# Performance work log

Measured on AMD Instinct MI355X. Metric: run time of the kernel, lower is better.

The kernel has to match this reference:

```python
import jax, jax.numpy as jnp
import numpy as np

NUM_HEADS = 16
HEAD_DIM = 80
DIM = NUM_HEADS * HEAD_DIM
SEQ = 2048
SCALE = HEAD_DIM ** -0.5


def rotate_half(x):
    x1, x2 = jnp.split(x, 2, axis=-1)
    return jnp.concatenate((-x2, x1), axis=-1)


def setup_inputs() -> dict:
    key = jax.random.key(0)
    ks = jax.random.split(key, 8)
    hidden_states = jax.random.normal(ks[0], (SEQ, DIM), dtype=jnp.float32)
    cu_seqlens = jnp.array([0, SEQ], dtype=jnp.int32)  # unused by the math
    # rotary embeddings for head_dim
    inv_freq = 1.0 / (10000.0 ** (jnp.arange(0, HEAD_DIM // 2, dtype=jnp.float32) / (HEAD_DIM // 2)))
    freqs = jnp.outer(jnp.arange(SEQ, dtype=jnp.float32), inv_freq)  # [S, hd/2]
    emb = jnp.concatenate((freqs, freqs), axis=-1)  # [S, hd]
    cos = jnp.cos(emb)
    sin = jnp.sin(emb)
    w_qkv = jax.random.normal(ks[1], (3 * DIM, DIM), dtype=jnp.float32) * (DIM ** -0.5)
    b_qkv = jax.random.normal(ks[2], (3 * DIM,), dtype=jnp.float32) * 0.02
    w_proj = jax.random.normal(ks[3], (DIM, DIM), dtype=jnp.float32) * (DIM ** -0.5)
    b_proj = jax.random.normal(ks[4], (DIM,), dtype=jnp.float32) * 0.02
    return {"hidden_states": hidden_states, "cu_seqlens": cu_seqlens, "cos": cos,
            "sin": sin, "w_qkv": w_qkv, "b_qkv": b_qkv, "w_proj": w_proj, "b_proj": b_proj}


def reference(hidden_states, cu_seqlens, cos, sin, w_qkv, b_qkv, w_proj, b_proj):
    S = hidden_states.shape[0]
    qkv = hidden_states @ w_qkv.T + b_qkv  # [S, 3*D]
    qkv = qkv.reshape(S, 3, NUM_HEADS, HEAD_DIM)
    q, k, v = qkv[:, 0], qkv[:, 1], qkv[:, 2]  # each [S, H, hd]
    c = cos[:, None, :]  # [S, 1, hd]
    s = sin[:, None, :]
    q = q * c + rotate_half(q) * s
    k = k * c + rotate_half(k) * s
    # SDPA, non-causal: [H, S, S]
    scores = jnp.einsum('shd,thd->hst', q, k) * SCALE
    attn = jax.nn.softmax(scores, axis=-1)
    out = jnp.einsum('hst,thd->shd', attn, v).reshape(S, DIM)
    return out @ w_proj.T + b_proj
```

## Files before the change

### kernel.cpp

```cpp
#include <hip/hip_runtime.h>


#define SEQLEN   2048
#define DIMM     1280
#define NHEADS   16
#define HD       80
#define HDP      96
#define QKV_N    3840
#define NSPLIT   2
#define KVSPAN   (SEQLEN / NSPLIT)
#define QSCALE_LOG2E 0.16130083587064776f

#define KSTRIDE  104
#define VSTRIDE  72
#define PSTRIDE  72

#define EXP2F(x) __builtin_amdgcn_exp2f(x)

#define GLD16(gptr, lptr)                                                      \
    __builtin_amdgcn_global_load_lds(                                          \
        (const __attribute__((address_space(1))) void*)(gptr),                 \
        (__attribute__((address_space(3))) void*)(lptr), 16, 0, 0)

typedef float f32x4 __attribute__((ext_vector_type(4)));
typedef _Float16 half8 __attribute__((ext_vector_type(8)));
typedef _Float16 half4 __attribute__((ext_vector_type(4)));

static __device__ __forceinline__ f32x4 mfma_16x16x32(half8 a, half8 b, f32x4 c) {
    return __builtin_amdgcn_mfma_f32_16x16x32_f16(a, b, c, 0, 0, 0);
}

__global__ void cast_f32_f16(const float* __restrict__ src,
                             _Float16* __restrict__ dst, int n4) {
    int i = blockIdx.x * blockDim.x + threadIdx.x;
    if (i < n4) {
        const float4 v = ((const float4*)src)[i];
        half4 h;
        h.x = (_Float16)v.x; h.y = (_Float16)v.y;
        h.z = (_Float16)v.z; h.w = (_Float16)v.w;
        ((half4*)dst)[i] = h;
    }
}

template<bool OUT_F16>
__global__ __launch_bounds__(256, 2)
void gemm_bt(const _Float16* __restrict__ A, const _Float16* __restrict__ B,
             const float* __restrict__ bias, void* __restrict__ Cout,
             int M, int N, int K) {
    __shared__ __align__(16) _Float16 As[128 * 32];
    __shared__ __align__(16) _Float16 Bs[128 * 32];
    const int tid  = threadIdx.x;
    const int lane = tid & 63;
    const int wave = tid >> 6;
    const int l15  = lane & 15;
    const int quad = lane >> 4;
    const int wm   = wave & 1;
    const int wn   = wave >> 1;
    const long bm = blockIdx.x, bn = blockIdx.y;

    const _Float16* Ag = A + bm * 128 * (long)K;
    const _Float16* Bg = B + bn * 128 * (long)K;

    const int srow = lane >> 2;
    const int scol = (lane & 3) * 8;
    f32x4 acc[4][4] = {};

    for (int k0 = 0; k0 < K; k0 += 32) {
        __syncthreads();
#pragma unroll
        for (int cc = 0; cc < 2; cc++) {
            const int c = wave + cc * 4;
            const long row = 16 * c + srow;
            GLD16(Ag + row * K + k0 + scol, As + 512 * c + lane * 8);
            GLD16(Bg + row * K + k0 + scol, Bs + 512 * c + lane * 8);
        }
        __syncthreads();
        half8 af[4], bf[4];
#pragma unroll
        for (int t = 0; t < 4; t++) {
            af[t] = *(const half8*)&As[(wm * 64 + t * 16 + l15) * 32 + quad * 8];
            bf[t] = *(const half8*)&Bs[(wn * 64 + t * 16 + l15) * 32 + quad * 8];
        }
#pragma unroll
        for (int mt = 0; mt < 4; mt++)
#pragma unroll
            for (int nt = 0; nt < 4; nt++)
                acc[mt][nt] = mfma_16x16x32(af[mt], bf[nt], acc[mt][nt]);
    }

    float bv[4];
#pragma unroll
    for (int nt = 0; nt < 4; nt++)
        bv[nt] = bias[bn * 128 + wn * 64 + nt * 16 + l15];

#pragma unroll
    for (int mt = 0; mt < 4; mt++) {
#pragma unroll
        for (int r = 0; r < 4; r++) {
            const long row = bm * 128 + wm * 64 + mt * 16 + quad * 4 + r;
#pragma unroll
            for (int nt = 0; nt < 4; nt++) {
                const long col = bn * 128 + wn * 64 + nt * 16 + l15;
                const float v = acc[mt][nt][r] + bv[nt];
                if (OUT_F16) ((_Float16*)Cout)[row * (long)N + col] = (_Float16)v;
                else         ((float*)Cout)[row * (long)N + col] = v;
            }
        }
    }
}

__global__ void rope_repack(const _Float16* __restrict__ qkv,
                            const float* __restrict__ cosb,
                            const float* __restrict__ sinb,
                            _Float16* __restrict__ Qh,
                            _Float16* __restrict__ Kh,
                            _Float16* __restrict__ Vh) {
    const int s = blockIdx.x;
    const int tid = threadIdx.x;
    const _Float16* row = qkv + (long)s * QKV_N;

    for (int i = tid; i < NHEADS * 40; i += 256) {
        const int h = i / 40, d = i - h * 40;
        const float c  = cosb[s * HD + d];
        const float sn = sinb[s * HD + d];
        const long o = ((long)h * SEQLEN + s) * HDP;
        const float q0 = (float)row[h * HD + d];
        const float q1 = (float)row[h * HD + d + 40];
        Qh[o + d]      = (_Float16)((q0 * c - q1 * sn) * QSCALE_LOG2E);
        Qh[o + d + 40] = (_Float16)((q1 * c + q0 * sn) * QSCALE_LOG2E);
        const float k0 = (float)row[DIMM + h * HD + d];
        const float k1 = (float)row[DIMM + h * HD + d + 40];
        Kh[o + d]      = (_Float16)(k0 * c - k1 * sn);
        Kh[o + d + 40] = (_Float16)(k1 * c + k0 * sn);
    }
    for (int i = tid; i < NHEADS * HD; i += 256) {
        const int h = i / HD, d = i - h * HD;
        Vh[((long)h * SEQLEN + s) * HDP + d] = row[2 * DIMM + i];
    }
    for (int i = tid; i < NHEADS * 16; i += 256) {
        const int h = i >> 4, d = HD + (i & 15);
        const long o = ((long)h * SEQLEN + s) * HDP + d;
        Qh[o] = (_Float16)0.f; Kh[o] = (_Float16)0.f;
    }
}

__global__ __launch_bounds__(256)
void v_transpose(const _Float16* __restrict__ Vh, _Float16* __restrict__ Vt) {
    const int s0 = blockIdx.x * 64;
    const int h  = blockIdx.y;
    __shared__ __align__(16) _Float16 Ts[64 * 88];
    const int tid = threadIdx.x;
    for (int i = tid; i < 640; i += 256) {
        const int r = i / 10, c = (i - r * 10) * 8;
        *(half8*)&Ts[r * 88 + c] =
            *(const half8*)&Vh[((long)h * SEQLEN + s0 + r) * HDP + c];
    }
    __syncthreads();
    for (int i = tid; i < 640; i += 256) {
        const int d = i >> 3, sc = (i & 7) * 8;
        half8 v;
#pragma unroll
        for (int j = 0; j < 8; j++) v[j] = Ts[(sc + j) * 88 + d];
        *(half8*)&Vt[((long)h * HD + d) * SEQLEN + s0 + sc] = v;
    }
}

__global__ __launch_bounds__(256, 4)
void attn_kernel(const _Float16* __restrict__ Qh, const _Float16* __restrict__ Kh,
                 const _Float16* __restrict__ Vt, _Float16* __restrict__ Ohat,
                 float* __restrict__ Lpart) {
    const int s0 = blockIdx.x * 64;
    const int h  = blockIdx.y;
    const int z  = blockIdx.z;
    __shared__ __align__(16) _Float16 Ks[64 * KSTRIDE];
    __shared__ __align__(16) _Float16 Vts[HD * VSTRIDE];
    __shared__ __align__(16) _Float16 Ps[4][16 * PSTRIDE];

    const int tid  = threadIdx.x;
    const int lane = tid & 63;
    const int wave = tid >> 6;
    const int l15  = lane & 15;
    const int quad = lane >> 4;

    const _Float16* Qg = Qh + ((long)h * SEQLEN + s0 + wave * 16 + l15) * HDP;
    half8 qf[3];
#pragma unroll
    for (int kk = 0; kk < 3; kk++)
        qf[kk] = *(const half8*)&Qg[kk * 32 + quad * 8];

    f32x4 oacc[5] = {};
    float l_r[4] = {0.f, 0.f, 0.f, 0.f};

    for (int t0 = z * KVSPAN; t0 < (z + 1) * KVSPAN; t0 += 64) {
        __syncthreads();
        const _Float16* Kg = Kh + ((long)h * SEQLEN + t0) * HDP;
        for (int i = tid; i < 768; i += 256) {
            const int r = i / 12, c = (i - r * 12) * 8;
            *(half8*)&Ks[r * KSTRIDE + c] = *(const half8*)&Kg[(long)r * HDP + c];
        }
        const _Float16* Vtg = Vt + (long)h * HD * SEQLEN + t0;
        for (int i = tid; i < 640; i += 256) {
            const int d = i >> 3, c = (i & 7) * 8;
            *(half8*)&Vts[d * VSTRIDE + c] = *(const half8*)&Vtg[(long)d * SEQLEN + c];
        }
        __syncthreads();

        f32x4 sa[4] = {};
#pragma unroll
        for (int kk = 0; kk < 3; kk++)
#pragma unroll
            for (int ct = 0; ct < 4; ct++) {
                half8 b = *(const half8*)&Ks[(ct * 16 + l15) * KSTRIDE + kk * 32 + quad * 8];
                sa[ct] = mfma_16x16x32(qf[kk], b, sa[ct]);
            }

        float p[4][4];
#pragma unroll
        for (int ct = 0; ct < 4; ct++)
#pragma unroll
            for (int r = 0; r < 4; r++) {
                p[ct][r] = EXP2F(sa[ct][r]);
                l_r[r] += p[ct][r];
                Ps[wave][(quad * 4 + r) * PSTRIDE + ct * 16 + l15] = (_Float16)p[ct][r];
            }
        asm volatile("s_waitcnt lgkmcnt(0)" ::: "memory");
        half8 pf0 = *(const half8*)&Ps[wave][l15 * PSTRIDE + quad * 8];
        half8 pf1 = *(const half8*)&Ps[wave][l15 * PSTRIDE + 32 + quad * 8];
#pragma unroll
        for (int nt = 0; nt < 5; nt++) {
            half8 v0 = *(const half8*)&Vts[(nt * 16 + l15) * VSTRIDE + quad * 8];
            half8 v1 = *(const half8*)&Vts[(nt * 16 + l15) * VSTRIDE + 32 + quad * 8];
            oacc[nt] = mfma_16x16x32(pf0, v0, oacc[nt]);
            oacc[nt] = mfma_16x16x32(pf1, v1, oacc[nt]);
        }
    }

#pragma unroll
    for (int off = 1; off < 16; off <<= 1)
#pragma unroll
        for (int r = 0; r < 4; r++)
            l_r[r] += __shfl_xor(l_r[r], off);

    float inv[4];
#pragma unroll
    for (int r = 0; r < 4; r++) inv[r] = 1.0f / l_r[r];

    const long base = ((long)z * NHEADS + h) * SEQLEN;
#pragma unroll
    for (int nt = 0; nt < 5; nt++)
#pragma unroll
        for (int r = 0; r < 4; r++) {
            const long row = s0 + wave * 16 + quad * 4 + r;
            Ohat[(base + row) * HD + nt * 16 + l15] = (_Float16)(oacc[nt][r] * inv[r]);
        }
    if (l15 == 0)
#pragma unroll
        for (int r = 0; r < 4; r++)
            Lpart[base + s0 + wave * 16 + quad * 4 + r] = l_r[r];
}

__global__ __launch_bounds__(256)
void attn_combine(const _Float16* __restrict__ Ohat, const float* __restrict__ Lp,
                  _Float16* __restrict__ attnb) {
    const int i = blockIdx.x * 256 + threadIdx.x;
    if (i >= SEQLEN * DIMM / 4) return;
    const int flat = i * 4;
    const int s = flat / DIMM;
    const int rem = flat - s * DIMM;
    const int h = rem / HD;
    const int d = rem - h * HD;
    const float l0 = Lp[h * SEQLEN + s];
    const float l1 = Lp[(NHEADS + h) * SEQLEN + s];
    const float invl = 1.0f / (l0 + l1);
    const float w0 = l0 * invl, w1 = l1 * invl;
    const half4 o0 = *(const half4*)&Ohat[((long)h * SEQLEN + s) * HD + d];
    const half4 o1 = *(const half4*)&Ohat[((long)(NHEADS + h) * SEQLEN + s) * HD + d];
    half4 o;
#pragma unroll
    for (int j = 0; j < 4; j++)
        o[j] = (_Float16)((float)o0[j] * w0 + (float)o1[j] * w1);
    *(half4*)&attnb[(long)s * DIMM + rem] = o;
}

extern "C" void kernel_launch(void* const* d_in, const int* in_sizes, int n_in,
                              void* d_out, int out_size, void* d_ws, size_t ws_size,
                              hipStream_t stream) {
    const float* hs     = (const float*)d_in[0];
    const float* cosb   = (const float*)d_in[2];
    const float* sinb   = (const float*)d_in[3];
    const float* w_qkv  = (const float*)d_in[4];
    const float* b_qkv  = (const float*)d_in[5];
    const float* w_proj = (const float*)d_in[6];
    const float* b_proj = (const float*)d_in[7];
    float* out = (float*)d_out;

    _Float16* hsb    = (_Float16*)d_ws;
    _Float16* wqkvb  = hsb    + (long)SEQLEN * DIMM;
    _Float16* wprojb = wqkvb  + (long)QKV_N * DIMM;
    _Float16* qkv    = wprojb + (long)DIMM * DIMM;
    _Float16* Qh     = qkv    + (long)SEQLEN * QKV_N;
    _Float16* Kh     = Qh     + (long)NHEADS * SEQLEN * HDP;
    _Float16* Vh     = Kh     + (long)NHEADS * SEQLEN * HDP;
    _Float16* Vtb    = Vh     + (long)NHEADS * SEQLEN * HDP;
    _Float16* attnb  = Vtb    + (long)NHEADS * HD * SEQLEN;

    _Float16* OhatB  = (_Float16*)d_ws;
    float*    LpartB = (float*)(OhatB + (long)NSPLIT * NHEADS * SEQLEN * HD);

    {
        int n4 = SEQLEN * DIMM / 4;
        cast_f32_f16<<<(n4 + 255) / 256, 256, 0, stream>>>(hs, hsb, n4);
        n4 = QKV_N * DIMM / 4;
        cast_f32_f16<<<(n4 + 255) / 256, 256, 0, stream>>>(w_qkv, wqkvb, n4);
        n4 = DIMM * DIMM / 4;
        cast_f32_f16<<<(n4 + 255) / 256, 256, 0, stream>>>(w_proj, wprojb, n4);
    }

    gemm_bt<true><<<dim3(SEQLEN / 128, QKV_N / 128), 256, 0, stream>>>(
        hsb, wqkvb, b_qkv, qkv, SEQLEN, QKV_N, DIMM);

    rope_repack<<<SEQLEN, 256, 0, stream>>>(qkv, cosb, sinb, Qh, Kh, Vh);

    v_transpose<<<dim3(SEQLEN / 64, NHEADS), 256, 0, stream>>>(Vh, Vtb);

    attn_kernel<<<dim3(SEQLEN / 64, NHEADS, NSPLIT), 256, 0, stream>>>(
        Qh, Kh, Vtb, OhatB, LpartB);

    attn_combine<<<(SEQLEN * DIMM / 4 + 255) / 256, 256, 0, stream>>>(
        OhatB, LpartB, attnb);

    gemm_bt<false><<<dim3(SEQLEN / 128, DIMM / 128), 256, 0, stream>>>(
        attnb, wprojb, b_proj, out, SEQLEN, DIMM, DIMM);
}
```

Measured before the change: 232.0 us.

## Double attention query tile per block and split KV four ways

The attention kernel now uses 512-thread blocks covering 128 query rows. Each K/V tile staged in LDS is therefore shared by eight waves instead of four. The KV sequence is split into four partitions instead of two, which keeps the same block count, and the combine kernel merges four partial outputs. The extra partial-output storage reuses the dead qkv workspace buffer. The costs are more combine traffic and a tighter register budget from the new launch bounds, which could cause spills.

```diff
diff --git a/kernel.cpp b/kernel.cpp
--- a/kernel.cpp
+++ b/kernel.cpp
@@ -7,7 +7,7 @@
 #define HD       80
 #define HDP      96
 #define QKV_N    3840
-#define NSPLIT   2
+#define NSPLIT   4
 #define KVSPAN   (SEQLEN / NSPLIT)
 #define QSCALE_LOG2E 0.16130083587064776f
 
@@ -165,16 +165,17 @@
     }
 }
 
-__global__ __launch_bounds__(256, 4)
+__global__ __launch_bounds__(512, 6)
 void attn_kernel(const _Float16* __restrict__ Qh, const _Float16* __restrict__ Kh,
-                 const _Float16* __restrict__ Vt, _Float16* __restrict__ Ohat,
+                 const _Float16* __restrict__ Vt,
+                 _Float16* __restrict__ Ohat0, _Float16* __restrict__ Ohat1,
                  float* __restrict__ Lpart) {
-    const int s0 = blockIdx.x * 64;
+    const int s0 = blockIdx.x * 128;
     const int h  = blockIdx.y;
     const int z  = blockIdx.z;
     __shared__ __align__(16) _Float16 Ks[64 * KSTRIDE];
     __shared__ __align__(16) _Float16 Vts[HD * VSTRIDE];
-    __shared__ __align__(16) _Float16 Ps[4][16 * PSTRIDE];
+    __shared__ __align__(16) _Float16 Ps[8][16 * PSTRIDE];
 
     const int tid  = threadIdx.x;
     const int lane = tid & 63;
@@ -194,12 +195,12 @@
     for (int t0 = z * KVSPAN; t0 < (z + 1) * KVSPAN; t0 += 64) {
         __syncthreads();
         const _Float16* Kg = Kh + ((long)h * SEQLEN + t0) * HDP;
-        for (int i = tid; i < 768; i += 256) {
+        for (int i = tid; i < 768; i += 512) {
             const int r = i / 12, c = (i - r * 12) * 8;
             *(half8*)&Ks[r * KSTRIDE + c] = *(const half8*)&Kg[(long)r * HDP + c];
         }
         const _Float16* Vtg = Vt + (long)h * HD * SEQLEN + t0;
-        for (int i = tid; i < 640; i += 256) {
+        for (int i = tid; i < 640; i += 512) {
             const int d = i >> 3, c = (i & 7) * 8;
             *(half8*)&Vts[d * VSTRIDE + c] = *(const half8*)&Vtg[(long)d * SEQLEN + c];
         }
@@ -245,22 +246,26 @@
 #pragma unroll
     for (int r = 0; r < 4; r++) inv[r] = 1.0f / l_r[r];
 
-    const long base = ((long)z * NHEADS + h) * SEQLEN;
+    _Float16* Oz = (z < 2) ? Ohat0 : Ohat1;
+    const long obase = ((long)(z & 1) * NHEADS + h) * SEQLEN;
+    const long lbase = ((long)z * NHEADS + h) * SEQLEN;
 #pragma unroll
     for (int nt = 0; nt < 5; nt++)
 #pragma unroll
         for (int r = 0; r < 4; r++) {
             const long row = s0 + wave * 16 + quad * 4 + r;
-            Ohat[(base + row) * HD + nt * 16 + l15] = (_Float16)(oacc[nt][r] * inv[r]);
+            Oz[(obase + row) * HD + nt * 16 + l15] = (_Float16)(oacc[nt][r] * inv[r]);
         }
     if (l15 == 0)
 #pragma unroll
         for (int r = 0; r < 4; r++)
-            Lpart[base + s0 + wave * 16 + quad * 4 + r] = l_r[r];
+            Lpart[lbase + s0 + wave * 16 + quad * 4 + r] = l_r[r];
 }
 
 __global__ __launch_bounds__(256)
-void attn_combine(const _Float16* __restrict__ Ohat, const float* __restrict__ Lp,
+void attn_combine(const _Float16* __restrict__ Ohat0,
+                  const _Float16* __restrict__ Ohat1,
+                  const float* __restrict__ Lp,
                   _Float16* __restrict__ attnb) {
     const int i = blockIdx.x * 256 + threadIdx.x;
     if (i >= SEQLEN * DIMM / 4) return;
@@ -269,16 +274,26 @@
     const int rem = flat - s * DIMM;
     const int h = rem / HD;
     const int d = rem - h * HD;
-    const float l0 = Lp[h * SEQLEN + s];
-    const float l1 = Lp[(NHEADS + h) * SEQLEN + s];
-    const float invl = 1.0f / (l0 + l1);
-    const float w0 = l0 * invl, w1 = l1 * invl;
-    const half4 o0 = *(const half4*)&Ohat[((long)h * SEQLEN + s) * HD + d];
-    const half4 o1 = *(const half4*)&Ohat[((long)(NHEADS + h) * SEQLEN + s) * HD + d];
+    float l[NSPLIT], lsum = 0.f;
+#pragma unroll
+    for (int zi = 0; zi < NSPLIT; zi++) {
+        l[zi] = Lp[((long)zi * NHEADS + h) * SEQLEN + s];
+        lsum += l[zi];
+    }
+    const float invl = 1.0f / lsum;
+    float acc[4] = {0.f, 0.f, 0.f, 0.f};
+#pragma unroll
+    for (int zi = 0; zi < NSPLIT; zi++) {
+        const _Float16* Oz = (zi < 2) ? Ohat0 : Ohat1;
+        const long obase = ((long)(zi & 1) * NHEADS + h) * SEQLEN;
+        const half4 o = *(const half4*)&Oz[(obase + s) * HD + d];
+        const float w = l[zi] * invl;
+#pragma unroll
+        for (int j = 0; j < 4; j++) acc[j] += (float)o[j] * w;
+    }
     half4 o;
 #pragma unroll
-    for (int j = 0; j < 4; j++)
-        o[j] = (_Float16)((float)o0[j] * w0 + (float)o1[j] * w1);
+    for (int j = 0; j < 4; j++) o[j] = (_Float16)acc[j];
     *(half4*)&attnb[(long)s * DIMM + rem] = o;
 }
 
@@ -304,8 +319,9 @@
     _Float16* Vtb    = Vh     + (long)NHEADS * SEQLEN * HDP;
     _Float16* attnb  = Vtb    + (long)NHEADS * HD * SEQLEN;
 
-    _Float16* OhatB  = (_Float16*)d_ws;
-    float*    LpartB = (float*)(OhatB + (long)NSPLIT * NHEADS * SEQLEN * HD);
+    _Float16* Ohat0  = (_Float16*)d_ws;
+    float*    LpartB = (float*)(Ohat0 + (long)2 * NHEADS * SEQLEN * HD);
+    _Float16* Ohat1  = qkv;
 
     {
         int n4 = SEQLEN * DIMM / 4;
@@ -323,11 +339,11 @@
 
     v_transpose<<<dim3(SEQLEN / 64, NHEADS), 256, 0, stream>>>(Vh, Vtb);
 
-    attn_kernel<<<dim3(SEQLEN / 64, NHEADS, NSPLIT), 256, 0, stream>>>(
-        Qh, Kh, Vtb, OhatB, LpartB);
+    attn_kernel<<<dim3(SEQLEN / 128, NHEADS, NSPLIT), 512, 0, stream>>>(
+        Qh, Kh, Vtb, Ohat0, Ohat1, LpartB);
 
     attn_combine<<<(SEQLEN * DIMM / 4 + 255) / 256, 256, 0, stream>>>(
-        OhatB, LpartB, attnb);
+        Ohat0, Ohat1, LpartB, attnb);
 
     gemm_bt<false><<<dim3(SEQLEN / 128, DIMM / 128), 256, 0, stream>>>(
         attnb, wprojb, b_proj, out, SEQLEN, DIMM, DIMM);
```

Measured after the change: 228.9 us. About the same (-1.3%).
